# Kernel tuning notes

Hardware: AMD Instinct MI355X
Metric: run time of the kernel (lower is better)

The kernel has to match this reference:

```python
import jax, jax.numpy as jnp
import numpy as np

NUM_EXPERTS = 8
K = 2
N_EMBD = 1024
HIDDEN = 4 * N_EMBD
BATCH = 2
SEQ = 1024
LB_SCALE = 0.01
NOISY_STD = 1.0
INIT_S = 0.02


def setup_inputs() -> dict:
    key = jax.random.key(0)
    ks = jax.random.split(key, 8)
    D, H, E = N_EMBD, HIDDEN, NUM_EXPERTS
    return {
        "x": jax.random.normal(ks[0], (BATCH, SEQ, D), jnp.float32),
        "noise": jax.random.normal(ks[1], (BATCH, SEQ, E), jnp.float32),  # torch.randn_like(logits)
        "gate_w": jax.random.normal(ks[2], (E, D), jnp.float32) * INIT_S,
        "noise_weight": jnp.zeros((E,), jnp.float32),  # initialized to zeros in the module
        "w1": jax.random.normal(ks[3], (E, H, D), jnp.float32) * INIT_S,
        "b1": jnp.zeros((E, H), jnp.float32),
        "w2": jax.random.normal(ks[4], (E, H, D), jnp.float32) * INIT_S,
        "b2": jnp.zeros((E, H), jnp.float32),
        "wp": jax.random.normal(ks[5], (E, D, H), jnp.float32) * INIT_S,
        "bp": jnp.zeros((E, D), jnp.float32),
    }


def reference(x, noise, gate_w, noise_weight, w1, b1, w2, b2, wp, bp):
    B, S, D = x.shape
    E = gate_w.shape[0]

    # ---- TopKGateParallel ----
    logits = jnp.einsum('bsd,ed->bse', x, gate_w)           # [B,S,E]
    gate_weights = jax.nn.softmax(logits, axis=-1)
    gw_mean = gate_weights.reshape(-1, E).mean(axis=0)       # [E]
    load_balance_loss = jnp.mean((gw_mean - 1.0 / E) ** 2) * LB_SCALE  # mse vs uniform

    logits_noisy = logits + (noise * NOISY_STD) * noise_weight
    top_v, top_i = jax.lax.top_k(logits_noisy, K)            # [B,S,K]
    # scatter top-k logits into a -inf sea, then softmax -> zeros at non-topk slots
    topk_mask = jnp.sum(jax.nn.one_hot(top_i, E, dtype=jnp.float32), axis=-2) > 0  # [B,S,E]
    sparse_logits = jnp.where(topk_mask, logits_noisy, -jnp.inf)
    top_k_gated_weights = jax.nn.softmax(sparse_logits, axis=-1)  # [B,S,E]

    # ---- expert compute + weighted combine (world_size=1: all experts local) ----
    x_flat = x.reshape(B * S, D)                              # [T,D]
    w_flat = top_k_gated_weights.reshape(B * S, E)            # [T,E]
    y = jnp.zeros_like(x_flat)
    for e in range(E):  # fixed small set of experts
        h = x_flat @ w1[e].T + b1[e]                          # [T,H]
        g = x_flat @ w2[e].T + b2[e]                          # [T,H]
        out_e = (h * jax.nn.silu(g)) @ wp[e].T + bp[e]        # [T,D]
        y = y + w_flat[:, e:e + 1] * out_e
    y = y.reshape(B, S, D)
    return y, load_balance_loss
```

## Files before the change

### kernel.cpp

```cpp
#include <hip/hip_runtime.h>

#define TOK 2048
#define DIM 1024
#define HID 4096
#define NE 8
#define KSPLIT 4
#define TMAX 24

typedef unsigned short u16;
typedef __attribute__((ext_vector_type(8))) short s16x8;
typedef __attribute__((ext_vector_type(4))) float f32x4;

__device__ __forceinline__ u16 f2b(float f) {
  unsigned u = __builtin_bit_cast(unsigned, f);
  unsigned r = (u + 0x7fffu + ((u >> 16) & 1u)) >> 16;
  return (u16)r;
}

__device__ __forceinline__ void gld_lds16(const void* g, void* l) {
  __builtin_amdgcn_global_load_lds((const __attribute__((address_space(1))) void*)g,
                                   (__attribute__((address_space(3))) void*)l, 16, 0, 0);
}

__global__ __launch_bounds__(256) void k_gate(const float* __restrict__ x,
    const float* __restrict__ noise, const float* __restrict__ gw,
    const float* __restrict__ nw, const float* __restrict__ w1,
    const float* __restrict__ w2, const float* __restrict__ wp,
    u16* __restrict__ w1b, u16* __restrict__ w2b, u16* __restrict__ wpb,
    int* __restrict__ tok_e, float* __restrict__ tok_w,
    int* __restrict__ bhist, float* __restrict__ bgw, u16* __restrict__ x16) {
  if (blockIdx.x >= TOK / 4) {
    const int cb = blockIdx.x - TOK / 4;
    const int tens = cb >> 8;
    const float* in = (tens == 0) ? w1 : (tens == 1) ? w2 : wp;
    u16* o = (tens == 0) ? w1b : (tens == 1) ? w2b : wpb;
    const size_t NPT = (size_t)NE * HID * DIM;
    const size_t stride = (size_t)256 * 256 * 8;
    for (size_t i = ((size_t)(cb & 255) * 256 + threadIdx.x) * 8; i < NPT; i += stride) {
      float4 a = *(const float4*)(in + i);
      float4 b = *(const float4*)(in + i + 4);
      u16 u[8];
      u[0] = f2b(a.x); u[1] = f2b(a.y); u[2] = f2b(a.z); u[3] = f2b(a.w);
      u[4] = f2b(b.x); u[5] = f2b(b.y); u[6] = f2b(b.z); u[7] = f2b(b.w);
      *(s16x8*)(o + i) = *(const s16x8*)u;
    }
    return;
  }
  const int wid = threadIdx.x >> 6, lane = threadIdx.x & 63;
  const int t = blockIdx.x * 4 + wid;
  const float* xr = x + (size_t)t * DIM + lane * 16;
  float acc[NE];
#pragma unroll
  for (int e = 0; e < NE; ++e) acc[e] = 0.f;
  u16 xb[16];
#pragma unroll
  for (int j = 0; j < 4; ++j) {
    float4 xv = *(const float4*)(xr + j * 4);
    xb[j * 4 + 0] = f2b(xv.x); xb[j * 4 + 1] = f2b(xv.y);
    xb[j * 4 + 2] = f2b(xv.z); xb[j * 4 + 3] = f2b(xv.w);
#pragma unroll
    for (int e = 0; e < NE; ++e) {
      float4 gv = *(const float4*)(gw + e * DIM + lane * 16 + j * 4);
      acc[e] += xv.x * gv.x + xv.y * gv.y + xv.z * gv.z + xv.w * gv.w;
    }
  }
  *(s16x8*)(x16 + (size_t)t * DIM + lane * 16) = *(const s16x8*)xb;
  *(s16x8*)(x16 + (size_t)t * DIM + lane * 16 + 8) = *(const s16x8*)(xb + 8);
#pragma unroll
  for (int e = 0; e < NE; ++e) {
#pragma unroll
    for (int off = 32; off >= 1; off >>= 1) acc[e] += __shfl_xor(acc[e], off);
  }
  float m = acc[0];
#pragma unroll
  for (int e = 1; e < NE; ++e) m = fmaxf(m, acc[e]);
  float p[NE]; float s = 0.f;
#pragma unroll
  for (int e = 0; e < NE; ++e) { p[e] = expf(acc[e] - m); s += p[e]; }
  float inv = 1.f / s;
  float v[NE];
#pragma unroll
  for (int e = 0; e < NE; ++e) v[e] = acc[e] + noise[t * NE + e] * nw[e];
  float v0 = -3.4e38f, v1 = -3.4e38f; int i0 = 0, i1 = 0;
#pragma unroll
  for (int e = 0; e < NE; ++e) {
    float ve = v[e];
    if (ve > v0) { v1 = v0; i1 = i0; v0 = ve; i0 = e; }
    else if (ve > v1) { v1 = ve; i1 = e; }
  }
  float e1 = expf(v1 - v0);
  float den = 1.f + e1;
  float w0 = 1.f / den, w1v = e1 / den;

  __shared__ float pl[4][NE];
  __shared__ int el[4][2];
  if (lane == 0) {
#pragma unroll
    for (int e = 0; e < NE; ++e) pl[wid][e] = p[e] * inv;
    el[wid][0] = i0; el[wid][1] = i1;
    tok_e[t * 2] = i0; tok_e[t * 2 + 1] = i1;
    tok_w[t * 2] = w0; tok_w[t * 2 + 1] = w1v;
  }
  __syncthreads();
  if (threadIdx.x < NE) {
    const int e = threadIdx.x;
    float ps = pl[0][e] + pl[1][e] + pl[2][e] + pl[3][e];
    int h = 0;
#pragma unroll
    for (int j = 0; j < 4; ++j) {
      h += (el[j][0] == e);
      h += (el[j][1] == e);
    }
    bgw[blockIdx.x * NE + e] = ps;
    bhist[blockIdx.x * NE + e] = h;
  }
}

__global__ __launch_bounds__(512) void k_scan(const int* __restrict__ bhist,
    const float* __restrict__ bgw, int* __restrict__ blk_off, int* __restrict__ prefix,
    int* __restrict__ counts, int* __restrict__ tile_tab, float* __restrict__ loss_out) {
  const int i = threadIdx.x, lane = i & 63, wv = i >> 6;
  __shared__ int wsum[8];
  __shared__ float wfs[8];
  __shared__ int etot[8];
  __shared__ float fsum[8];
  for (int e = 0; e < NE; ++e) {
    int v = bhist[i * NE + e];
    int sc = v;
#pragma unroll
    for (int off = 1; off < 64; off <<= 1) {
      int u = __shfl_up(sc, off);
      if (lane >= off) sc += u;
    }
    float f = bgw[i * NE + e];
#pragma unroll
    for (int off = 32; off >= 1; off >>= 1) f += __shfl_xor(f, off);
    if (lane == 63) wsum[wv] = sc;
    if (lane == 0) wfs[wv] = f;
    __syncthreads();
    int base = 0;
    for (int w2 = 0; w2 < wv; ++w2) base += wsum[w2];
    blk_off[i * NE + e] = base + sc - v;
    if (i == 0) {
      float tf = 0.f;
      for (int w2 = 0; w2 < 8; ++w2) tf += wfs[w2];
      fsum[e] = tf;
    }
    if (i == 511) etot[e] = base + sc;
    __syncthreads();
  }
  if (i == 0) {
    int sacc = 0;
    float l = 0.f;
    int tt = 0;
#pragma unroll
    for (int e = 0; e < NE; ++e) { prefix[e] = sacc; counts[e] = etot[e]; sacc += etot[e]; }
    for (int e = 0; e < NE; ++e) {
      const int nmt = (etot[e] + 255) >> 8;
      for (int m2 = 0; m2 < nmt; ++m2) tile_tab[tt++] = (e << 16) | m2;
    }
    for (; tt < TMAX; ++tt) tile_tab[tt] = -1;
#pragma unroll
    for (int e = 0; e < NE; ++e) {
      float d = fsum[e] * (1.f / TOK) - 0.125f;
      l += d * d;
    }
    *loss_out = l * (0.01f / NE);
  }
}

__global__ __launch_bounds__(256) void k_build(const int* __restrict__ tok_e,
    const float* __restrict__ tok_w, const int* __restrict__ prefix,
    const int* __restrict__ blk_off, int* __restrict__ ent, float* __restrict__ entw,
    int* __restrict__ inv) {
  const int t = blockIdx.x * 256 + threadIdx.x;
  const int g = t >> 2;
  const int base = (t & 3) * 2;
  int ee[8];
#pragma unroll
  for (int j = 0; j < 8; ++j) ee[j] = tok_e[g * 8 + j];
#pragma unroll
  for (int s = 0; s < 2; ++s) {
    const int e = ee[base + s];
    int rank = 0;
#pragma unroll
    for (int j = 0; j < 8; ++j) rank += (j < base + s) && (ee[j] == e);
    const int idx = prefix[e] + blk_off[g * NE + e] + rank;
    ent[idx] = t * 2 + s;
    entw[idx] = tok_w[t * 2 + s];
    inv[t * 2 + s] = idx;
  }
}

__global__ __launch_bounds__(512) void k_gemm1f(const u16* __restrict__ x16,
    const u16* __restrict__ w1b, const u16* __restrict__ w2b,
    const float* __restrict__ b1, const float* __restrict__ b2,
    const int* __restrict__ ent, const int* __restrict__ counts,
    const int* __restrict__ prefix, const int* __restrict__ tile_tab,
    u16* __restrict__ act) {
  const int tt = tile_tab[blockIdx.y];
  if (tt < 0) return;
  const int e = tt >> 16, mt = tt & 0xffff, nt = blockIdx.x;
  const int cnt = counts[e];
  const int pfx = prefix[e];
  const int tid = threadIdx.x, w = tid >> 6, l = tid & 63;

  __shared__ u16 smem[2][16384];

  const int r0 = tid >> 2;
  const int c = (tid & 3) ^ ((tid >> 3) & 3);
  int g0 = mt * 256 + r0;       if (g0 >= cnt) g0 = cnt - 1;
  int g1 = mt * 256 + 128 + r0; if (g1 >= cnt) g1 = cnt - 1;
  const u16* sa0 = x16 + (size_t)(ent[pfx + g0] >> 1) * DIM + c * 8;
  const u16* sa1 = x16 + (size_t)(ent[pfx + g1] >> 1) * DIM + c * 8;
  const u16* sb1 = w1b + ((size_t)e * HID + nt * 128 + r0) * DIM + c * 8;
  const u16* sb2 = w2b + ((size_t)e * HID + nt * 128 + r0) * DIM + c * 8;
  const int oA0 = tid * 8, oA1 = 4096 + tid * 8;
  const int oB1 = 8192 + tid * 8, oB2 = 12288 + tid * 8;

  const int wr = w >> 1, wc = w & 1;
  const int xs = ((l >> 4) ^ ((l >> 1) & 3)) * 8;
  const int ra = (wr * 64 + (l & 15)) * 32 + xs;
  const int rb = (wc * 64 + (l & 15)) * 32 + xs;

  f32x4 acc1[4][4], acc2[4][4];
#pragma unroll
  for (int m = 0; m < 4; ++m)
#pragma unroll
    for (int n = 0; n < 4; ++n) {
      acc1[m][n] = (f32x4){0.f, 0.f, 0.f, 0.f};
      acc2[m][n] = (f32x4){0.f, 0.f, 0.f, 0.f};
    }

  auto STAGE = [&](int buf, int k0) {
    gld_lds16(sa0 + k0, &smem[buf][oA0]);
    gld_lds16(sa1 + k0, &smem[buf][oA1]);
    gld_lds16(sb1 + k0, &smem[buf][oB1]);
    gld_lds16(sb2 + k0, &smem[buf][oB2]);
  };

  STAGE(0, 0);
  __syncthreads();
  int cur = 0;
  for (int kt = 0; kt < DIM / 32; ++kt) {
    if (kt < DIM / 32 - 1) STAGE(cur ^ 1, (kt + 1) * 32);
    const u16* S = &smem[cur][0];
    s16x8 af[4];
#pragma unroll
    for (int m = 0; m < 4; ++m) af[m] = *(const s16x8*)(S + ra + m * 512);
#pragma unroll
    for (int n = 0; n < 4; ++n) {
      s16x8 bf1 = *(const s16x8*)(S + 8192 + rb + n * 512);
      s16x8 bf2 = *(const s16x8*)(S + 12288 + rb + n * 512);
#pragma unroll
      for (int m = 0; m < 4; ++m) {
        acc1[m][n] = __builtin_amdgcn_mfma_f32_16x16x32_bf16(af[m], bf1, acc1[m][n], 0, 0, 0);
        acc2[m][n] = __builtin_amdgcn_mfma_f32_16x16x32_bf16(af[m], bf2, acc2[m][n], 0, 0, 0);
      }
    }
    __syncthreads();
    cur ^= 1;
  }

#pragma unroll
  for (int n = 0; n < 4; ++n) {
    const int col = nt * 128 + wc * 64 + n * 16 + (l & 15);
    const float bb1 = b1[(size_t)e * HID + col];
    const float bb2 = b2[(size_t)e * HID + col];
#pragma unroll
    for (int m = 0; m < 4; ++m) {
#pragma unroll
      for (int r = 0; r < 4; ++r) {
        const int row = mt * 256 + wr * 64 + m * 16 + (l >> 4) * 4 + r;
        if (row < cnt) {
          float h = acc1[m][n][r] + bb1;
          float g = acc2[m][n][r] + bb2;
          float a = h * g / (1.f + expf(-g));
          act[(size_t)(pfx + row) * HID + col] = f2b(a);
        }
      }
    }
  }
}

__global__ __launch_bounds__(512) void k_gemm2f(const u16* __restrict__ act,
    const u16* __restrict__ wpb, const float* __restrict__ bp,
    const float* __restrict__ entw, const int* __restrict__ counts,
    const int* __restrict__ prefix, const int* __restrict__ tile_tab,
    float* __restrict__ yp) {
  const int tt = tile_tab[blockIdx.y];
  if (tt < 0) return;
  const int e = tt >> 16, mt = tt & 0xffff;
  const int sk = blockIdx.z, nt = blockIdx.x;
  const int cnt = counts[e];
  const int pfx = prefix[e];
  const int tid = threadIdx.x, w = tid >> 6, l = tid & 63;

  __shared__ u16 smem[2][16384];

  const int r0 = tid >> 2;
  const int c = (tid & 3) ^ ((tid >> 3) & 3);
  int g0 = mt * 256 + r0;       if (g0 >= cnt) g0 = cnt - 1;
  int g1 = mt * 256 + 128 + r0; if (g1 >= cnt) g1 = cnt - 1;
  const int kbase = sk * (HID / KSPLIT);
  const u16* sa0 = act + (size_t)(pfx + g0) * HID + kbase + c * 8;
  const u16* sa1 = act + (size_t)(pfx + g1) * HID + kbase + c * 8;
  const u16* sb0 = wpb + ((size_t)e * DIM + nt * 256 + r0) * HID + kbase + c * 8;
  const u16* sb1 = sb0 + (size_t)128 * HID;
  const int oA0 = tid * 8, oA1 = 4096 + tid * 8;
  const int oB0 = 8192 + tid * 8, oB1 = 12288 + tid * 8;

  const int wr = w >> 2, wc = w & 3;
  const int xs = ((l >> 4) ^ ((l >> 1) & 3)) * 8;
  const int ra = (wr * 128 + (l & 15)) * 32 + xs;
  const int rb = 8192 + (wc * 64 + (l & 15)) * 32 + xs;

  f32x4 acc[8][4];
#pragma unroll
  for (int m = 0; m < 8; ++m)
#pragma unroll
    for (int n = 0; n < 4; ++n) acc[m][n] = (f32x4){0.f, 0.f, 0.f, 0.f};

  auto STAGE = [&](int buf, int k0) {
    gld_lds16(sa0 + k0, &smem[buf][oA0]);
    gld_lds16(sa1 + k0, &smem[buf][oA1]);
    gld_lds16(sb0 + k0, &smem[buf][oB0]);
    gld_lds16(sb1 + k0, &smem[buf][oB1]);
  };

  STAGE(0, 0);
  __syncthreads();
  int cur = 0;
  const int NIT = HID / KSPLIT / 32;
  for (int kt = 0; kt < NIT; ++kt) {
    if (kt < NIT - 1) STAGE(cur ^ 1, (kt + 1) * 32);
    const u16* S = &smem[cur][0];
#pragma unroll
    for (int n = 0; n < 4; ++n) {
      s16x8 bf = *(const s16x8*)(S + rb + n * 512);
#pragma unroll
      for (int m = 0; m < 8; ++m) {
        s16x8 af = *(const s16x8*)(S + ra + m * 512);
        acc[m][n] = __builtin_amdgcn_mfma_f32_16x16x32_bf16(af, bf, acc[m][n], 0, 0, 0);
      }
    }
    __syncthreads();
    cur ^= 1;
  }

#pragma unroll
  for (int n = 0; n < 4; ++n) {
    const int col = nt * 256 + wc * 64 + n * 16 + (l & 15);
    const float bpv = (sk == 0) ? bp[(size_t)e * DIM + col] : 0.f;
#pragma unroll
    for (int m = 0; m < 8; ++m) {
#pragma unroll
      for (int r = 0; r < 4; ++r) {
        const int row = mt * 256 + wr * 128 + m * 16 + (l >> 4) * 4 + r;
        if (row < cnt) {
          const int idx = pfx + row;
          yp[((size_t)sk * (TOK * 2) + idx) * DIM + col] = entw[idx] * (acc[m][n][r] + bpv);
        }
      }
    }
  }
}

__global__ __launch_bounds__(256) void k_final(const float* __restrict__ yp,
    const int* __restrict__ inv, float* __restrict__ out) {
  const int t = blockIdx.x;
  const int d = threadIdx.x * 4;
  const int i0 = inv[t * 2], i1 = inv[t * 2 + 1];
  float4 s = {0.f, 0.f, 0.f, 0.f};
#pragma unroll
  for (int sk = 0; sk < KSPLIT; ++sk) {
    float4 a = *(const float4*)(yp + ((size_t)sk * (TOK * 2) + i0) * DIM + d);
    float4 b = *(const float4*)(yp + ((size_t)sk * (TOK * 2) + i1) * DIM + d);
    s.x += a.x + b.x; s.y += a.y + b.y; s.z += a.z + b.z; s.w += a.w + b.w;
  }
  *(float4*)(out + (size_t)t * DIM + d) = s;
}

extern "C" void kernel_launch(void* const* d_in, const int* in_sizes, int n_in,
                              void* d_out, int out_size, void* d_ws, size_t ws_size,
                              hipStream_t stream) {
  const float* x      = (const float*)d_in[0];
  const float* noise  = (const float*)d_in[1];
  const float* gate_w = (const float*)d_in[2];
  const float* nw     = (const float*)d_in[3];
  const float* w1     = (const float*)d_in[4];
  const float* b1     = (const float*)d_in[5];
  const float* w2     = (const float*)d_in[6];
  const float* b2     = (const float*)d_in[7];
  const float* wp     = (const float*)d_in[8];
  const float* bp     = (const float*)d_in[9];
  float* out = (float*)d_out;
  char* ws = (char*)d_ws;

  const size_t SZ_X16 = (size_t)TOK * DIM * 2;
  const size_t SZ_ACT = (size_t)TOK * 2 * HID * 2;
  const size_t SZ_W   = (size_t)NE * HID * DIM * 2;

  u16* x16 = (u16*)ws;
  u16* act = (u16*)(ws + SZ_X16);
  u16* w1b = (u16*)(ws + SZ_X16 + SZ_ACT);
  u16* w2b = (u16*)(ws + SZ_X16 + SZ_ACT + SZ_W);
  u16* wpb = (u16*)(ws + SZ_X16 + SZ_ACT + 2 * SZ_W);
  float* yp = (float*)w1b;
  char* meta = ws + SZ_X16 + SZ_ACT + 3 * SZ_W;
  int*   tok_e    = (int*)(meta);
  float* tok_w    = (float*)(meta + 16384);
  int*   ent      = (int*)(meta + 32768);
  float* entw     = (float*)(meta + 49152);
  int*   bhist    = (int*)(meta + 65536);
  float* bgw      = (float*)(meta + 81920);
  int*   blk_off  = (int*)(meta + 98304);
  int*   inv      = (int*)(meta + 114688);
  int*   counts   = (int*)(meta + 131072);
  int*   prefix   = (int*)(meta + 131072 + 64);
  int*   tile_tab = (int*)(meta + 131072 + 128);

  k_gate<<<TOK / 4 + 768, 256, 0, stream>>>(x, noise, gate_w, nw, w1, w2, wp,
                                            w1b, w2b, wpb, tok_e, tok_w, bhist, bgw, x16);
  k_scan<<<1, 512, 0, stream>>>(bhist, bgw, blk_off, prefix, counts, tile_tab,
                                out + (size_t)TOK * DIM);
  k_build<<<TOK / 256, 256, 0, stream>>>(tok_e, tok_w, prefix, blk_off, ent, entw, inv);
  k_gemm1f<<<dim3(HID / 128, TMAX), 512, 0, stream>>>(x16, w1b, w2b, b1, b2, ent,
                                                      counts, prefix, tile_tab, act);
  k_gemm2f<<<dim3(DIM / 256, TMAX, KSPLIT), 512, 0, stream>>>(act, wpb, bp, entw,
                                                              counts, prefix, tile_tab, yp);
  k_final<<<TOK, 256, 0, stream>>>(yp, inv, out);
}
```

Baseline: 384.2 us.

## Prefetch two K-stages ahead in expert GEMMs and widen weight-cast grid

After: 387.6 us. About the same (+0.9%).

```diff
diff --git a/kernel.cpp b/kernel.cpp
--- a/kernel.cpp
+++ b/kernel.cpp
@@ -6,6 +6,7 @@
 #define NE 8
 #define KSPLIT 4
 #define TMAX 24
+#define NCAST 2048
 
 typedef unsigned short u16;
 typedef __attribute__((ext_vector_type(8))) short s16x8;
@@ -31,18 +32,19 @@
     int* __restrict__ bhist, float* __restrict__ bgw, u16* __restrict__ x16) {
   if (blockIdx.x >= TOK / 4) {
     const int cb = blockIdx.x - TOK / 4;
-    const int tens = cb >> 8;
-    const float* in = (tens == 0) ? w1 : (tens == 1) ? w2 : wp;
-    u16* o = (tens == 0) ? w1b : (tens == 1) ? w2b : wpb;
     const size_t NPT = (size_t)NE * HID * DIM;
-    const size_t stride = (size_t)256 * 256 * 8;
-    for (size_t i = ((size_t)(cb & 255) * 256 + threadIdx.x) * 8; i < NPT; i += stride) {
-      float4 a = *(const float4*)(in + i);
-      float4 b = *(const float4*)(in + i + 4);
+    const size_t stride = (size_t)NCAST * 256 * 8;
+    for (size_t i = ((size_t)cb * 256 + threadIdx.x) * 8; i < 3 * NPT; i += stride) {
+      const float* in; u16* o; size_t j;
+      if (i < NPT)          { in = w1; o = w1b; j = i; }
+      else if (i < 2 * NPT) { in = w2; o = w2b; j = i - NPT; }
+      else                  { in = wp; o = wpb; j = i - 2 * NPT; }
+      float4 a = *(const float4*)(in + j);
+      float4 b = *(const float4*)(in + j + 4);
       u16 u[8];
       u[0] = f2b(a.x); u[1] = f2b(a.y); u[2] = f2b(a.z); u[3] = f2b(a.w);
       u[4] = f2b(b.x); u[5] = f2b(b.y); u[6] = f2b(b.z); u[7] = f2b(b.w);
-      *(s16x8*)(o + i) = *(const s16x8*)u;
+      *(s16x8*)(o + j) = *(const s16x8*)u;
     }
     return;
   }
@@ -239,11 +241,14 @@
     gld_lds16(sb2 + k0, &smem[buf][oB2]);
   };
 
+  const int NT = DIM / 32;
   STAGE(0, 0);
-  __syncthreads();
+  STAGE(1, 32);
+  asm volatile("s_waitcnt vmcnt(4)" ::: "memory");
+  __builtin_amdgcn_s_barrier();
+  __builtin_amdgcn_sched_barrier(0);
   int cur = 0;
-  for (int kt = 0; kt < DIM / 32; ++kt) {
-    if (kt < DIM / 32 - 1) STAGE(cur ^ 1, (kt + 1) * 32);
+  for (int kt = 0; kt < NT; ++kt) {
     const u16* S = &smem[cur][0];
     s16x8 af[4];
 #pragma unroll
@@ -258,7 +263,19 @@
         acc2[m][n] = __builtin_amdgcn_mfma_f32_16x16x32_bf16(af[m], bf2, acc2[m][n], 0, 0, 0);
       }
     }
-    __syncthreads();
+    if (kt + 1 < NT) {
+      asm volatile("s_waitcnt lgkmcnt(0)" ::: "memory");
+      __builtin_amdgcn_sched_barrier(0);
+      __builtin_amdgcn_s_barrier();
+      if (kt + 2 < NT) {
+        STAGE(cur, (kt + 2) * 32);
+        asm volatile("s_waitcnt vmcnt(4)" ::: "memory");
+      } else {
+        asm volatile("s_waitcnt vmcnt(0)" ::: "memory");
+      }
+      __builtin_amdgcn_s_barrier();
+      __builtin_amdgcn_sched_barrier(0);
+    }
     cur ^= 1;
   }
 
@@ -328,12 +345,14 @@
     gld_lds16(sb1 + k0, &smem[buf][oB1]);
   };
 
+  const int NIT = HID / KSPLIT / 32;
   STAGE(0, 0);
-  __syncthreads();
+  STAGE(1, 32);
+  asm volatile("s_waitcnt vmcnt(4)" ::: "memory");
+  __builtin_amdgcn_s_barrier();
+  __builtin_amdgcn_sched_barrier(0);
   int cur = 0;
-  const int NIT = HID / KSPLIT / 32;
   for (int kt = 0; kt < NIT; ++kt) {
-    if (kt < NIT - 1) STAGE(cur ^ 1, (kt + 1) * 32);
     const u16* S = &smem[cur][0];
 #pragma unroll
     for (int n = 0; n < 4; ++n) {
@@ -344,7 +363,19 @@
         acc[m][n] = __builtin_amdgcn_mfma_f32_16x16x32_bf16(af, bf, acc[m][n], 0, 0, 0);
       }
     }
-    __syncthreads();
+    if (kt + 1 < NIT) {
+      asm volatile("s_waitcnt lgkmcnt(0)" ::: "memory");
+      __builtin_amdgcn_sched_barrier(0);
+      __builtin_amdgcn_s_barrier();
+      if (kt + 2 < NIT) {
+        STAGE(cur, (kt + 2) * 32);
+        asm volatile("s_waitcnt vmcnt(4)" ::: "memory");
+      } else {
+        asm volatile("s_waitcnt vmcnt(0)" ::: "memory");
+      }
+      __builtin_amdgcn_s_barrier();
+      __builtin_amdgcn_sched_barrier(0);
+    }
     cur ^= 1;
   }
 
@@ -420,8 +451,8 @@
   int*   prefix   = (int*)(meta + 131072 + 64);
   int*   tile_tab = (int*)(meta + 131072 + 128);
 
-  k_gate<<<TOK / 4 + 768, 256, 0, stream>>>(x, noise, gate_w, nw, w1, w2, wp,
-                                            w1b, w2b, wpb, tok_e, tok_w, bhist, bgw, x16);
+  k_gate<<<TOK / 4 + NCAST, 256, 0, stream>>>(x, noise, gate_w, nw, w1, w2, wp,
+                                              w1b, w2b, wpb, tok_e, tok_w, bhist, bgw, x16);
   k_scan<<<1, 512, 0, stream>>>(bhist, bgw, blk_off, prefix, counts, tile_tab,
                                 out + (size_t)TOK * DIM);
   k_build<<<TOK / 256, 256, 0, stream>>>(tok_e, tok_w, prefix, blk_off, ent, entw, inv);
```
